# Kernel optimization log

Measured on AMD Instinct MI355X. Metric: run time of the kernel, lower is better.

## Reference

```python
import jax, jax.numpy as jnp
import numpy as np

B, T, D, H, O = 64, 512, 64, 512, 64

def setup_inputs() -> dict:
    key = jax.random.key(0)
    ks = jax.random.split(key, 12)
    s = lambda fan: 1.0 / np.sqrt(fan)
    return {
        "x": jax.random.normal(ks[0], (B, T, D), jnp.float32),
        "W_ih0": jax.random.normal(ks[1], (4 * H, D), jnp.float32) * s(D),
        "W_hh0": jax.random.normal(ks[2], (4 * H, H), jnp.float32) * s(H),
        "b_ih0": jax.random.normal(ks[3], (4 * H,), jnp.float32) * s(H),
        "b_hh0": jax.random.normal(ks[4], (4 * H,), jnp.float32) * s(H),
        "W_ih1": jax.random.normal(ks[5], (4 * H, H), jnp.float32) * s(H),
        "W_hh1": jax.random.normal(ks[6], (4 * H, H), jnp.float32) * s(H),
        "b_ih1": jax.random.normal(ks[7], (4 * H,), jnp.float32) * s(H),
        "b_hh1": jax.random.normal(ks[8], (4 * H,), jnp.float32) * s(H),
        "lin_w": jax.random.normal(ks[9], (O, H), jnp.float32) * s(H),
        "lin_b": jax.random.normal(ks[10], (O,), jnp.float32) * s(H),
    }

def _lstm_layer(x_seq, h0, c0, W_ih, W_hh, b_ih, b_hh):
    # Precompute input contribution for all timesteps: [B, T, 4H]
    xg = jnp.einsum('btd,gd->btg', x_seq, W_ih) + b_ih
    def step(carry, xg_t):
        h, c = carry
        gates = xg_t + h @ W_hh.T + b_hh  # [B, 4H]
        i, f, g, o = jnp.split(gates, 4, axis=-1)
        i = jax.nn.sigmoid(i); f = jax.nn.sigmoid(f)
        g = jnp.tanh(g); o = jax.nn.sigmoid(o)
        c = f * c + i * g  # eval mode: dropout mask is identity
        h = o * jnp.tanh(c)
        return (h, c), h
    (h, c), ys = jax.lax.scan(step, (h0, c0), jnp.swapaxes(xg, 0, 1))
    return jnp.swapaxes(ys, 0, 1), h, c

def reference(x, W_ih0, W_hh0, b_ih0, b_hh0, W_ih1, W_hh1, b_ih1, b_hh1, lin_w, lin_b):
    h = jnp.zeros((x.shape[0], H), x.dtype)
    c = jnp.zeros((x.shape[0], H), x.dtype)
    # NOTE: faithful to source — h/c are only zeroed before layer 0 and
    # carried into layer 1 as its initial state.
    y0, h, c = _lstm_layer(x, h, c, W_ih0, W_hh0, b_ih0, b_hh0)
    y1, h, c = _lstm_layer(y0, h, c, W_ih1, W_hh1, b_ih1, b_hh1)
    return h @ lin_w.T + lin_b  # [B, O]
```

## Files before the change

### kernel.cpp

```cpp
#include <hip/hip_runtime.h>

#define TSEQ 512

typedef unsigned short us8v __attribute__((ext_vector_type(8)));
typedef __bf16 bf16x8 __attribute__((ext_vector_type(8)));
typedef float f32x4 __attribute__((ext_vector_type(4)));
typedef unsigned u32x4 __attribute__((ext_vector_type(4)));

#define OFF_BIAS  0u
#define OFF_X16   16384u
#define OFF_W0    4210688u
#define OFF_W1    6569984u
#define OFF_Y0P   10764288u
#define OFF_RING0 44318720u
#define OFF_RING1 44580864u
#define OFF_HFIN  44843008u

static __device__ __forceinline__ unsigned short f2bf(float f) {
    unsigned u = __builtin_bit_cast(unsigned, f);
    u += 0x7fffu + ((u >> 16) & 1u);
    return (unsigned short)(u >> 16);
}
static __device__ __forceinline__ float sigmf(float x) { return 1.0f / (1.0f + __expf(-x)); }
static __device__ __forceinline__ float tanh_fast(float x) {
    float a = fabsf(x);
    float e = __expf(-2.0f * a);
    float t = (1.0f - e) / (1.0f + e);
    return copysignf(t, x);
}
static __device__ __forceinline__ f32x4 mfma16(us8v a, us8v b, f32x4 c) {
    return __builtin_amdgcn_mfma_f32_16x16x32_bf16(
        __builtin_bit_cast(bf16x8, a), __builtin_bit_cast(bf16x8, b), c, 0, 0, 0);
}
static __device__ __forceinline__ bool fresh8(u32x4 a,u32x4 b,u32x4 c,u32x4 d,
                                              u32x4 e,u32x4 f,u32x4 g,u32x4 h,unsigned ep) {
    unsigned x = (a[3]^ep)|(b[3]^ep)|(c[3]^ep)|(d[3]^ep)|(e[3]^ep)|(f[3]^ep)|(g[3]^ep)|(h[3]^ep);
    return __all((int)(x == 0u));
}

__global__ void setup_kernel(const float* __restrict__ x,
                             const float* __restrict__ wih0, const float* __restrict__ whh0,
                             const float* __restrict__ bih0, const float* __restrict__ bhh0,
                             const float* __restrict__ wih1, const float* __restrict__ whh1,
                             const float* __restrict__ bih1, const float* __restrict__ bhh1,
                             char* __restrict__ ws)
{
    unsigned idx = blockIdx.x * blockDim.x + threadIdx.x;
    unsigned stride = gridDim.x * blockDim.x;
    unsigned short* x16 = (unsigned short*)(ws + OFF_X16);
    unsigned short* w0  = (unsigned short*)(ws + OFF_W0);
    unsigned short* w1  = (unsigned short*)(ws + OFF_W1);
    float* bias = (float*)(ws + OFF_BIAS);
    const unsigned NX  = 64u*512u*64u;
    const unsigned NW0 = 2048u*576u;
    const unsigned NW1 = 2048u*1024u;
    const unsigned NT  = NX + NW0 + NW1 + 4096u;
    for (unsigned i = idx; i < NT; i += stride) {
        if (i < NX) {
            unsigned d = i & 63u, b = (i >> 6) & 63u, t = i >> 12;
            x16[i] = f2bf(x[((b << 9) + t) * 64u + d]);
        } else if (i < NX + NW0) {
            unsigned k = i - NX; unsigned r = k / 576u, c = k % 576u;
            float v = (c < 64u) ? wih0[r*64u + c] : whh0[r*512u + (c - 64u)];
            w0[k] = f2bf(v);
        } else if (i < NX + NW0 + NW1) {
            unsigned k = i - NX - NW0; unsigned r = k >> 10, c = k & 1023u;
            float v = (c < 512u) ? wih1[(r<<9) + c] : whh1[(r<<9) + (c - 512u)];
            w1[k] = f2bf(v);
        } else {
            unsigned k = i - NX - NW0 - NW1;
            float v = (k < 2048u) ? (bih0[k] + bhh0[k]) : (bih1[k-2048u] + bhh1[k-2048u]);
            bias[k] = v;
        }
    }
}

__launch_bounds__(256, 1)
__global__ void lstm_persist(char* __restrict__ ws)
{
    const int tid  = threadIdx.x;
    const int kq   = tid >> 6;
    const int lane = tid & 63;
    const int l15  = lane & 15;
    const int lhi  = lane >> 4;
    const int bg   = blockIdx.x & 3;
    const int hg   = blockIdx.x >> 2;

    const float* bias = (const float*)(ws + OFF_BIAS);
    const char*  x16  = ws + OFF_X16;
    char* y0p   = ws + OFF_Y0P;
    char* ring0 = ws + OFF_RING0;
    char* ring1 = ws + OFF_RING1;

    __shared__ __align__(16) char arena[86016];
    float* gsum   = (float*)arena;
    float* bias_l = (float*)(arena + 35840);

    if (tid < 64) bias_l[tid] = bias[(tid >> 4)*512 + hg*16 + (tid & 15)];

    float cst = 0.0f;
    const int b_ = tid >> 4, p_ = tid & 15;

    us8v A[4][8];
    {
        const char* w0p = ws + OFF_W0;
        #pragma unroll
        for (int m = 0; m < 4; ++m) {
            const char* base = w0p + (size_t)(m*512 + hg*16 + l15)*1152 + lhi*16;
            #pragma unroll
            for (int kk = 0; kk < 4; ++kk)
                A[m][kk] = *(const us8v*)(base + (2 + kq*4 + kk)*64);
            if (kq < 2) A[m][4] = *(const us8v*)(base + kq*64);
        }
    }
    __syncthreads();

    const int vo_a   = kq*8192 + (lhi>>1)*1024 + l15*64 + (lhi&1)*32;
    const int vo_b   = vo_a + 4096;
    const int vo_x   = l15*128 + (kq & 1)*64 + lhi*16;
    const int vo_y   = kq*4096 + (lhi>>1)*512 + l15*32 + (lhi&1)*16;
    const int vo_tag = b_*64 + (p_ & 3)*16;
    const int vo_pl  = b_*32 + (p_ & 1)*16;

    u32x4 c0,c1,c2,c3,c4,c5,c6,c7;

#define LOAD8(SB)                                                               \
    asm volatile(                                                               \
        "global_load_dwordx4 %0, %8, %10 sc0 sc1\n\t"                           \
        "global_load_dwordx4 %1, %8, %10 offset:16 sc0 sc1\n\t"                 \
        "global_load_dwordx4 %2, %8, %10 offset:2048 sc0 sc1\n\t"               \
        "global_load_dwordx4 %3, %8, %10 offset:2064 sc0 sc1\n\t"               \
        "global_load_dwordx4 %4, %9, %10 sc0 sc1\n\t"                           \
        "global_load_dwordx4 %5, %9, %10 offset:16 sc0 sc1\n\t"                 \
        "global_load_dwordx4 %6, %9, %10 offset:2048 sc0 sc1\n\t"               \
        "global_load_dwordx4 %7, %9, %10 offset:2064 sc0 sc1\n\t"               \
        "s_waitcnt vmcnt(0)"                                                    \
        : "=&v"(c0),"=&v"(c1),"=&v"(c2),"=&v"(c3),                              \
          "=&v"(c4),"=&v"(c5),"=&v"(c6),"=&v"(c7)                               \
        : "v"(vo_a), "v"(vo_b), "s"(SB) : "memory")

#define LOAD8X(SB, XR, SBX)                                                     \
    asm volatile(                                                               \
        "global_load_dwordx4 %8, %11, %12\n\t"                                  \
        "global_load_dwordx4 %0, %9, %13 sc0 sc1\n\t"                           \
        "global_load_dwordx4 %1, %9, %13 offset:16 sc0 sc1\n\t"                 \
        "global_load_dwordx4 %2, %9, %13 offset:2048 sc0 sc1\n\t"               \
        "global_load_dwordx4 %3, %9, %13 offset:2064 sc0 sc1\n\t"               \
        "global_load_dwordx4 %4, %10, %13 sc0 sc1\n\t"                          \
        "global_load_dwordx4 %5, %10, %13 offset:16 sc0 sc1\n\t"                \
        "global_load_dwordx4 %6, %10, %13 offset:2048 sc0 sc1\n\t"              \
        "global_load_dwordx4 %7, %10, %13 offset:2064 sc0 sc1\n\t"              \
        "s_waitcnt vmcnt(0)"                                                    \
        : "=&v"(c0),"=&v"(c1),"=&v"(c2),"=&v"(c3),                              \
          "=&v"(c4),"=&v"(c5),"=&v"(c6),"=&v"(c7), "=&v"(XR)                    \
        : "v"(vo_a), "v"(vo_b), "v"(vo_x), "s"(SBX), "s"(SB) : "memory")

#define LOAD8Y(SB, SBY)                                                         \
    asm volatile(                                                               \
        "global_load_dwordx4 %8, %14, %15\n\t"                                  \
        "global_load_dwordx4 %9, %14, %15 offset:1024\n\t"                      \
        "global_load_dwordx4 %10, %14, %15 offset:2048\n\t"                     \
        "global_load_dwordx4 %11, %14, %15 offset:3072\n\t"                     \
        "global_load_dwordx4 %0, %12, %16 sc0 sc1\n\t"                          \
        "global_load_dwordx4 %1, %12, %16 offset:16 sc0 sc1\n\t"                \
        "global_load_dwordx4 %2, %12, %16 offset:2048 sc0 sc1\n\t"              \
        "global_load_dwordx4 %3, %12, %16 offset:2064 sc0 sc1\n\t"              \
        "global_load_dwordx4 %4, %13, %16 sc0 sc1\n\t"                          \
        "global_load_dwordx4 %5, %13, %16 offset:16 sc0 sc1\n\t"                \
        "global_load_dwordx4 %6, %13, %16 offset:2048 sc0 sc1\n\t"              \
        "global_load_dwordx4 %7, %13, %16 offset:2064 sc0 sc1\n\t"              \
        "s_waitcnt vmcnt(0)"                                                    \
        : "=&v"(c0),"=&v"(c1),"=&v"(c2),"=&v"(c3),                              \
          "=&v"(c4),"=&v"(c5),"=&v"(c6),"=&v"(c7),                              \
          "=&v"(yr0),"=&v"(yr1),"=&v"(yr2),"=&v"(yr3)                           \
        : "v"(vo_a), "v"(vo_b), "v"(vo_y), "s"(SBY), "s"(SB) : "memory")

#define FRAG(a,b) __builtin_bit_cast(us8v, (u32x4){(a)[0],(a)[1],(b)[0],(b)[1]})

#define GSUM_WRITE(PAR)                                                           \
    do {                                                                          \
        float* gs_ = gsum + (PAR)*4352;                                           \
        _Pragma("unroll")                                                         \
        for (int m = 0; m < 4; ++m) {                                             \
            _Pragma("unroll")                                                     \
            for (int q = 0; q < 4; ++q)                                           \
                gs_[(m*16 + lhi*4 + q)*68 + kq*17 + l15] = acc[m][q];             \
        }                                                                         \
    } while (0)

#define ACT_STEP(PAR, EPS, SBTAG, DOPLAIN, SBPL)                                  \
    do {                                                                          \
        const float* gsr = gsum + (PAR)*4352;                                     \
        float g4[4];                                                              \
        _Pragma("unroll")                                                         \
        for (int g = 0; g < 4; ++g) {                                             \
            float s = bias_l[g*16 + p_];                                          \
            _Pragma("unroll")                                                     \
            for (int kk = 0; kk < 4; ++kk) s += gsr[(g*16 + p_)*68 + kk*17 + b_]; \
            g4[g] = s;                                                            \
        }                                                                         \
        float iv = sigmf(g4[0]), fv = sigmf(g4[1]);                               \
        float gv = tanh_fast(g4[2]), ov = sigmf(g4[3]);                           \
        cst = fv*cst + iv*gv;                                                     \
        float hh = ov * tanh_fast(cst);                                           \
        unsigned hv = f2bf(hh);                                                   \
        unsigned pk = (hv & 0xffffu) | (((unsigned)__shfl_xor((int)hv,1)) << 16); \
        int rbx = lane & 48;                                                      \
        unsigned Da = (unsigned)__shfl((int)pk, rbx + (p_&3)*4);                  \
        unsigned Db = (unsigned)__shfl((int)pk, rbx + (p_&3)*4 + 2);              \
        unsigned P0 = (unsigned)__shfl((int)pk, rbx + (p_&1)*8);                  \
        unsigned P1 = (unsigned)__shfl((int)pk, rbx + (p_&1)*8 + 2);              \
        unsigned P2 = (unsigned)__shfl((int)pk, rbx + (p_&1)*8 + 4);              \
        unsigned P3 = (unsigned)__shfl((int)pk, rbx + (p_&1)*8 + 6);              \
        if (p_ < 4) {                                                             \
            u32x4 tu = {Da, Db, 0u, (EPS)};                                       \
            asm volatile("global_store_dwordx4 %0, %1, %2 sc0 sc1"                \
                         :: "v"(vo_tag), "v"(tu), "s"(SBTAG) : "memory");         \
        }                                                                         \
        if ((DOPLAIN) && (p_ == 4 || p_ == 5)) {                                  \
            u32x4 pu = {P0, P1, P2, P3};                                          \
            asm volatile("global_store_dwordx4 %0, %1, %2 sc0 sc1"                \
                         :: "v"(vo_pl), "v"(pu), "s"(SBPL) : "memory");           \
        }                                                                         \
    } while (0)

    for (int t = 0; t < TSEQ; ++t) {
        const int par = t & 1;
        const char* sbx = x16 + (size_t)t*8192 + bg*2048;
        u32x4 xr;
        f32x4 acc[4] = {{0.f,0.f,0.f,0.f},{0.f,0.f,0.f,0.f},{0.f,0.f,0.f,0.f},{0.f,0.f,0.f,0.f}};
        if (t > 0) {
            const char* sbr = ring0 + ((size_t)((t-1)&1)*4 + bg)*32768;
            const unsigned ep = (unsigned)t;
            LOAD8X(sbr, xr, sbx);
            while (!fresh8(c0,c1,c2,c3,c4,c5,c6,c7, ep)) LOAD8(sbr);
            if (kq < 2) {
                #pragma unroll
                for (int m = 0; m < 4; ++m)
                    acc[m] = mfma16(A[m][4], __builtin_bit_cast(us8v, xr), acc[m]);
            }
            us8v h0 = FRAG(c0,c1), h1 = FRAG(c2,c3), h2 = FRAG(c4,c5), h3 = FRAG(c6,c7);
            #pragma unroll
            for (int m = 0; m < 4; ++m) acc[m] = mfma16(A[m][0], h0, acc[m]);
            #pragma unroll
            for (int m = 0; m < 4; ++m) acc[m] = mfma16(A[m][1], h1, acc[m]);
            #pragma unroll
            for (int m = 0; m < 4; ++m) acc[m] = mfma16(A[m][2], h2, acc[m]);
            #pragma unroll
            for (int m = 0; m < 4; ++m) acc[m] = mfma16(A[m][3], h3, acc[m]);
        } else {
            asm volatile("global_load_dwordx4 %0, %1, %2\n\ts_waitcnt vmcnt(0)"
                         : "=&v"(xr) : "v"(vo_x), "s"(sbx) : "memory");
            if (kq < 2) {
                #pragma unroll
                for (int m = 0; m < 4; ++m)
                    acc[m] = mfma16(A[m][4], __builtin_bit_cast(us8v, xr), acc[m]);
            }
        }
        GSUM_WRITE(par);
        __syncthreads();
        const char* sbt = ring0 + ((size_t)par*4 + bg)*32768 + hg*1024;
        const char* sbp = y0p + ((size_t)t*4 + bg)*16384 + hg*512;
        ACT_STEP(par, (unsigned)(t + 1), sbt, 1, sbp);
    }

    __syncthreads();
    {
        const char* w1p = ws + OFF_W1;
        #pragma unroll
        for (int m = 0; m < 4; ++m) {
            const char* base = w1p + (size_t)(m*512 + hg*16 + l15)*2048 + lhi*16;
            #pragma unroll
            for (int kk = 0; kk < 4; ++kk) {
                A[m][kk]     = *(const us8v*)(base + (kq*4 + kk)*64);
                A[m][kk + 4] = *(const us8v*)(base + (16 + kq*4 + kk)*64);
            }
        }
    }
    if (tid < 64) bias_l[tid] = bias[2048 + (tid >> 4)*512 + hg*16 + (tid & 15)];
    __syncthreads();

    for (int t = 0; t < TSEQ; ++t) {
        const int par = t & 1;
        const char* sby = y0p + ((size_t)t*4 + bg)*16384;
        const char* sbr = (t == 0) ? (ring0 + ((size_t)1*4 + bg)*32768)
                                   : (ring1 + ((size_t)((t-1)&1)*4 + bg)*32768);
        const unsigned ep = (unsigned)(512 + t);
        u32x4 yr0, yr1, yr2, yr3;
        LOAD8Y(sbr, sby);
        while (!fresh8(c0,c1,c2,c3,c4,c5,c6,c7, ep)) LOAD8(sbr);

        f32x4 acc[4] = {{0.f,0.f,0.f,0.f},{0.f,0.f,0.f,0.f},{0.f,0.f,0.f,0.f},{0.f,0.f,0.f,0.f}};
        #pragma unroll
        for (int m = 0; m < 4; ++m) acc[m] = mfma16(A[m][0], __builtin_bit_cast(us8v, yr0), acc[m]);
        #pragma unroll
        for (int m = 0; m < 4; ++m) acc[m] = mfma16(A[m][1], __builtin_bit_cast(us8v, yr1), acc[m]);
        #pragma unroll
        for (int m = 0; m < 4; ++m) acc[m] = mfma16(A[m][2], __builtin_bit_cast(us8v, yr2), acc[m]);
        #pragma unroll
        for (int m = 0; m < 4; ++m) acc[m] = mfma16(A[m][3], __builtin_bit_cast(us8v, yr3), acc[m]);
        {
            us8v h0 = FRAG(c0,c1), h1 = FRAG(c2,c3), h2 = FRAG(c4,c5), h3 = FRAG(c6,c7);
            #pragma unroll
            for (int m = 0; m < 4; ++m) acc[m] = mfma16(A[m][4], h0, acc[m]);
            #pragma unroll
            for (int m = 0; m < 4; ++m) acc[m] = mfma16(A[m][5], h1, acc[m]);
            #pragma unroll
            for (int m = 0; m < 4; ++m) acc[m] = mfma16(A[m][6], h2, acc[m]);
            #pragma unroll
            for (int m = 0; m < 4; ++m) acc[m] = mfma16(A[m][7], h3, acc[m]);
        }
        GSUM_WRITE(par);
        __syncthreads();
        const char* sbt = ring1 + ((size_t)par*4 + bg)*32768 + hg*1024;
        const char* sbp = ws + OFF_HFIN + ((size_t)bg*32 + hg)*512;
        ACT_STEP(par, (unsigned)(513 + t), sbt, (t == 511), sbp);
    }
#undef LOAD8
#undef LOAD8X
#undef LOAD8Y
#undef FRAG
#undef GSUM_WRITE
#undef ACT_STEP
}

__global__ void final_linear(const char* __restrict__ ws,
                             const float* __restrict__ linw, const float* __restrict__ linb,
                             float* __restrict__ out)
{
    __shared__ float hrow[512];
    int b = blockIdx.x;
    int o = threadIdx.x;
    int bg = b >> 4, bl = b & 15;
    const char* src = ws + OFF_HFIN + ((size_t)bg*32 + (o >> 1))*512 + bl*32 + (o & 1)*16;
    {
        us8v v = *(const us8v*)src;
        #pragma unroll
        for (int p = 0; p < 8; ++p)
            hrow[o*8+p] = __builtin_bit_cast(float, ((unsigned)v[p]) << 16);
    }
    __syncthreads();
    float acc = linb[o];
    const float* wrow = linw + o*512;
    #pragma unroll 8
    for (int k = 0; k < 512; ++k) acc += hrow[k] * wrow[k];
    out[b*64 + o] = acc;
}

extern "C" void kernel_launch(void* const* d_in, const int* in_sizes, int n_in,
                              void* d_out, int out_size, void* d_ws, size_t ws_size,
                              hipStream_t stream)
{
    const float* x    = (const float*)d_in[0];
    const float* wih0 = (const float*)d_in[1];
    const float* whh0 = (const float*)d_in[2];
    const float* bih0 = (const float*)d_in[3];
    const float* bhh0 = (const float*)d_in[4];
    const float* wih1 = (const float*)d_in[5];
    const float* whh1 = (const float*)d_in[6];
    const float* bih1 = (const float*)d_in[7];
    const float* bih1_ = bih1;  (void)bih1_;
    const float* bhh1 = (const float*)d_in[8];
    const float* linw = (const float*)d_in[9];
    const float* linb = (const float*)d_in[10];
    char* ws = (char*)d_ws;

    (void)hipMemsetAsync(ws + OFF_RING0, 0, 262144u*2 + 65536u, stream);
    hipLaunchKernelGGL(setup_kernel, dim3(1024), dim3(256), 0, stream,
                       x, wih0, whh0, bih0, bhh0, wih1, whh1, bih1, bhh1, ws);
    hipLaunchKernelGGL(lstm_persist, dim3(128), dim3(256), 0, stream, ws);
    hipLaunchKernelGGL(final_linear, dim3(64), dim3(64), 0, stream,
                       ws, linw, linb, (float*)d_out);
}
```

Before: 2.489 ms.

## Halve persistent grid and replace tagged ring polling with per-group flag counters

The persistent LSTM kernel moves from 128 to 64 blocks, with each block owning 32 hidden units (8 MFMA row tiles) instead of 16. Cross-block hidden-state exchange no longer polls epoch tags embedded in every 16-byte payload. It now uses plain h buffers plus a small per-batch-group flag array, polled with a tight inline-asm loop, and layer-0 outputs are read directly from y0p. This is meant to cut the number of blocks that must synchronise each timestep and the polling traffic, at the cost of twice as much MFMA and activation work per block and more registers for the weights.

After: 3.195 ms. 28.4% more time.

```diff
diff --git a/kernel.cpp b/kernel.cpp
--- a/kernel.cpp
+++ b/kernel.cpp
@@ -12,9 +12,8 @@
 #define OFF_W0    4210688u
 #define OFF_W1    6569984u
 #define OFF_Y0P   10764288u
-#define OFF_RING0 44318720u
-#define OFF_RING1 44580864u
-#define OFF_HFIN  44843008u
+#define OFF_RING1 44318720u
+#define OFF_FLAGS 44449792u
 
 static __device__ __forceinline__ unsigned short f2bf(float f) {
     unsigned u = __builtin_bit_cast(unsigned, f);
@@ -32,11 +31,7 @@
     return __builtin_amdgcn_mfma_f32_16x16x32_bf16(
         __builtin_bit_cast(bf16x8, a), __builtin_bit_cast(bf16x8, b), c, 0, 0, 0);
 }
-static __device__ __forceinline__ bool fresh8(u32x4 a,u32x4 b,u32x4 c,u32x4 d,
-                                              u32x4 e,u32x4 f,u32x4 g,u32x4 h,unsigned ep) {
-    unsigned x = (a[3]^ep)|(b[3]^ep)|(c[3]^ep)|(d[3]^ep)|(e[3]^ep)|(f[3]^ep)|(g[3]^ep)|(h[3]^ep);
-    return __all((int)(x == 0u));
-}
+static __device__ __forceinline__ us8v asb(u32x4 v) { return __builtin_bit_cast(us8v, v); }
 
 __global__ void setup_kernel(const float* __restrict__ x,
                              const float* __restrict__ wih0, const float* __restrict__ whh0,
@@ -89,24 +84,27 @@
     const float* bias = (const float*)(ws + OFF_BIAS);
     const char*  x16  = ws + OFF_X16;
     char* y0p   = ws + OFF_Y0P;
-    char* ring0 = ws + OFF_RING0;
     char* ring1 = ws + OFF_RING1;
+    char* flags = ws + OFF_FLAGS;
 
     __shared__ __align__(16) char arena[86016];
     float* gsum   = (float*)arena;
-    float* bias_l = (float*)(arena + 35840);
-
-    if (tid < 64) bias_l[tid] = bias[(tid >> 4)*512 + hg*16 + (tid & 15)];
-
-    float cst = 0.0f;
-    const int b_ = tid >> 4, p_ = tid & 15;
-
-    us8v A[4][8];
+    float* bias_l = (float*)(arena + 70656);
+    unsigned* wcnt = (unsigned*)(arena + 71680);
+
+    if (tid == 0) { wcnt[0] = 0u; wcnt[1] = 0u; }
+    if (tid < 128) bias_l[tid] = bias[(tid >> 5)*512 + hg*32 + (tid & 31)];
+
+    const int b_ = tid >> 4, p0 = (tid & 15) * 2;
+    float cs0 = 0.0f, cs1 = 0.0f;
+
+    us8v A[8][8];
     {
         const char* w0p = ws + OFF_W0;
         #pragma unroll
-        for (int m = 0; m < 4; ++m) {
-            const char* base = w0p + (size_t)(m*512 + hg*16 + l15)*1152 + lhi*16;
+        for (int m = 0; m < 8; ++m) {
+            const char* base = w0p
+                + (size_t)((m >> 1)*512 + hg*32 + (m & 1)*16 + l15)*1152 + lhi*16;
             #pragma unroll
             for (int kk = 0; kk < 4; ++kk)
                 A[m][kk] = *(const us8v*)(base + (2 + kq*4 + kk)*64);
@@ -115,161 +113,168 @@
     }
     __syncthreads();
 
-    const int vo_a   = kq*8192 + (lhi>>1)*1024 + l15*64 + (lhi&1)*32;
-    const int vo_b   = vo_a + 4096;
-    const int vo_x   = l15*128 + (kq & 1)*64 + lhi*16;
-    const int vo_y   = kq*4096 + (lhi>>1)*512 + l15*32 + (lhi&1)*16;
-    const int vo_tag = b_*64 + (p_ & 3)*16;
-    const int vo_pl  = b_*32 + (p_ & 1)*16;
-
-    u32x4 c0,c1,c2,c3,c4,c5,c6,c7;
-
-#define LOAD8(SB)                                                               \
+    const int vo_h = kq*4096 + l15*64 + lhi*16;
+    const int vo_x = (bg*16 + l15)*128 + (kq & 1)*64 + lhi*16;
+    const char* fp = flags + bg*2048 + (lane & 15)*128;
+    const char* fq = flags + bg*2048 + hg*128;
+
+    u32x4 xr, yr0, yr1, yr2, yr3, h0, h1, h2, h3;
+
+#define POLL_L0(SBX, EP)                                                        \
+    do { unsigned pf0_, pf1_, ep_ = (EP);                                       \
     asm volatile(                                                               \
-        "global_load_dwordx4 %0, %8, %10 sc0 sc1\n\t"                           \
-        "global_load_dwordx4 %1, %8, %10 offset:16 sc0 sc1\n\t"                 \
-        "global_load_dwordx4 %2, %8, %10 offset:2048 sc0 sc1\n\t"               \
-        "global_load_dwordx4 %3, %8, %10 offset:2064 sc0 sc1\n\t"               \
-        "global_load_dwordx4 %4, %9, %10 sc0 sc1\n\t"                           \
-        "global_load_dwordx4 %5, %9, %10 offset:16 sc0 sc1\n\t"                 \
-        "global_load_dwordx4 %6, %9, %10 offset:2048 sc0 sc1\n\t"               \
-        "global_load_dwordx4 %7, %9, %10 offset:2064 sc0 sc1\n\t"               \
+        "global_load_dwordx4 %0, %3, %4\n\t"                                    \
+        "global_load_dword %1, %5, off sc0 sc1\n\t"                             \
+        "global_load_dword %2, %5, off sc0 sc1\n\t"                             \
+        "1:\n\t"                                                                \
+        "s_waitcnt vmcnt(1)\n\t"                                                \
+        "v_cmp_lt_u32 vcc, %1, %6\n\t"                                          \
+        "s_cbranch_vccz 2f\n\t"                                                 \
+        "global_load_dword %1, %5, off sc0 sc1\n\t"                             \
+        "s_waitcnt vmcnt(1)\n\t"                                                \
+        "v_cmp_lt_u32 vcc, %2, %6\n\t"                                          \
+        "s_cbranch_vccz 2f\n\t"                                                 \
+        "global_load_dword %2, %5, off sc0 sc1\n\t"                             \
+        "s_branch 1b\n\t"                                                       \
+        "2:\n\t"                                                                \
         "s_waitcnt vmcnt(0)"                                                    \
-        : "=&v"(c0),"=&v"(c1),"=&v"(c2),"=&v"(c3),                              \
-          "=&v"(c4),"=&v"(c5),"=&v"(c6),"=&v"(c7)                               \
-        : "v"(vo_a), "v"(vo_b), "s"(SB) : "memory")
-
-#define LOAD8X(SB, XR, SBX)                                                     \
+        : "=&v"(xr), "=&v"(pf0_), "=&v"(pf1_)                                   \
+        : "v"(vo_x), "s"(SBX), "v"(fp), "v"(ep_)                                \
+        : "vcc", "memory"); } while (0)
+
+#define POLL_L1(SBY, EP)                                                        \
+    do { unsigned pf0_, pf1_, ep_ = (EP);                                       \
     asm volatile(                                                               \
-        "global_load_dwordx4 %8, %11, %12\n\t"                                  \
-        "global_load_dwordx4 %0, %9, %13 sc0 sc1\n\t"                           \
-        "global_load_dwordx4 %1, %9, %13 offset:16 sc0 sc1\n\t"                 \
-        "global_load_dwordx4 %2, %9, %13 offset:2048 sc0 sc1\n\t"               \
-        "global_load_dwordx4 %3, %9, %13 offset:2064 sc0 sc1\n\t"               \
-        "global_load_dwordx4 %4, %10, %13 sc0 sc1\n\t"                          \
-        "global_load_dwordx4 %5, %10, %13 offset:16 sc0 sc1\n\t"                \
-        "global_load_dwordx4 %6, %10, %13 offset:2048 sc0 sc1\n\t"              \
-        "global_load_dwordx4 %7, %10, %13 offset:2064 sc0 sc1\n\t"              \
+        "global_load_dwordx4 %0, %6, %7\n\t"                                    \
+        "global_load_dwordx4 %1, %6, %7 offset:1024\n\t"                        \
+        "global_load_dwordx4 %2, %6, %7 offset:2048\n\t"                        \
+        "global_load_dwordx4 %3, %6, %7 offset:3072\n\t"                        \
+        "global_load_dword %4, %8, off sc0 sc1\n\t"                             \
+        "global_load_dword %5, %8, off sc0 sc1\n\t"                             \
+        "1:\n\t"                                                                \
+        "s_waitcnt vmcnt(1)\n\t"                                                \
+        "v_cmp_lt_u32 vcc, %4, %9\n\t"                                          \
+        "s_cbranch_vccz 2f\n\t"                                                 \
+        "global_load_dword %4, %8, off sc0 sc1\n\t"                             \
+        "s_waitcnt vmcnt(1)\n\t"                                                \
+        "v_cmp_lt_u32 vcc, %5, %9\n\t"                                          \
+        "s_cbranch_vccz 2f\n\t"                                                 \
+        "global_load_dword %5, %8, off sc0 sc1\n\t"                             \
+        "s_branch 1b\n\t"                                                       \
+        "2:\n\t"                                                                \
         "s_waitcnt vmcnt(0)"                                                    \
-        : "=&v"(c0),"=&v"(c1),"=&v"(c2),"=&v"(c3),                              \
-          "=&v"(c4),"=&v"(c5),"=&v"(c6),"=&v"(c7), "=&v"(XR)                    \
-        : "v"(vo_a), "v"(vo_b), "v"(vo_x), "s"(SBX), "s"(SB) : "memory")
-
-#define LOAD8Y(SB, SBY)                                                         \
+        : "=&v"(yr0), "=&v"(yr1), "=&v"(yr2), "=&v"(yr3), "=&v"(pf0_), "=&v"(pf1_) \
+        : "v"(vo_h), "s"(SBY), "v"(fp), "v"(ep_)                                \
+        : "vcc", "memory"); } while (0)
+
+#define LOADH4(SB)                                                              \
     asm volatile(                                                               \
-        "global_load_dwordx4 %8, %14, %15\n\t"                                  \
-        "global_load_dwordx4 %9, %14, %15 offset:1024\n\t"                      \
-        "global_load_dwordx4 %10, %14, %15 offset:2048\n\t"                     \
-        "global_load_dwordx4 %11, %14, %15 offset:3072\n\t"                     \
-        "global_load_dwordx4 %0, %12, %16 sc0 sc1\n\t"                          \
-        "global_load_dwordx4 %1, %12, %16 offset:16 sc0 sc1\n\t"                \
-        "global_load_dwordx4 %2, %12, %16 offset:2048 sc0 sc1\n\t"              \
-        "global_load_dwordx4 %3, %12, %16 offset:2064 sc0 sc1\n\t"              \
-        "global_load_dwordx4 %4, %13, %16 sc0 sc1\n\t"                          \
-        "global_load_dwordx4 %5, %13, %16 offset:16 sc0 sc1\n\t"                \
-        "global_load_dwordx4 %6, %13, %16 offset:2048 sc0 sc1\n\t"              \
-        "global_load_dwordx4 %7, %13, %16 offset:2064 sc0 sc1\n\t"              \
+        "global_load_dwordx4 %0, %4, %5\n\t"                                    \
+        "global_load_dwordx4 %1, %4, %5 offset:1024\n\t"                        \
+        "global_load_dwordx4 %2, %4, %5 offset:2048\n\t"                        \
+        "global_load_dwordx4 %3, %4, %5 offset:3072\n\t"                        \
         "s_waitcnt vmcnt(0)"                                                    \
-        : "=&v"(c0),"=&v"(c1),"=&v"(c2),"=&v"(c3),                              \
-          "=&v"(c4),"=&v"(c5),"=&v"(c6),"=&v"(c7),                              \
-          "=&v"(yr0),"=&v"(yr1),"=&v"(yr2),"=&v"(yr3)                           \
-        : "v"(vo_a), "v"(vo_b), "v"(vo_y), "s"(SBY), "s"(SB) : "memory")
-
-#define FRAG(a,b) __builtin_bit_cast(us8v, (u32x4){(a)[0],(a)[1],(b)[0],(b)[1]})
-
-#define GSUM_WRITE(PAR)                                                           \
-    do {                                                                          \
-        float* gs_ = gsum + (PAR)*4352;                                           \
-        _Pragma("unroll")                                                         \
-        for (int m = 0; m < 4; ++m) {                                             \
-            _Pragma("unroll")                                                     \
-            for (int q = 0; q < 4; ++q)                                           \
-                gs_[(m*16 + lhi*4 + q)*68 + kq*17 + l15] = acc[m][q];             \
-        }                                                                         \
-    } while (0)
-
-#define ACT_STEP(PAR, EPS, SBTAG, DOPLAIN, SBPL)                                  \
-    do {                                                                          \
-        const float* gsr = gsum + (PAR)*4352;                                     \
-        float g4[4];                                                              \
-        _Pragma("unroll")                                                         \
-        for (int g = 0; g < 4; ++g) {                                             \
-            float s = bias_l[g*16 + p_];                                          \
-            _Pragma("unroll")                                                     \
-            for (int kk = 0; kk < 4; ++kk) s += gsr[(g*16 + p_)*68 + kk*17 + b_]; \
-            g4[g] = s;                                                            \
-        }                                                                         \
-        float iv = sigmf(g4[0]), fv = sigmf(g4[1]);                               \
-        float gv = tanh_fast(g4[2]), ov = sigmf(g4[3]);                           \
-        cst = fv*cst + iv*gv;                                                     \
-        float hh = ov * tanh_fast(cst);                                           \
-        unsigned hv = f2bf(hh);                                                   \
-        unsigned pk = (hv & 0xffffu) | (((unsigned)__shfl_xor((int)hv,1)) << 16); \
-        int rbx = lane & 48;                                                      \
-        unsigned Da = (unsigned)__shfl((int)pk, rbx + (p_&3)*4);                  \
-        unsigned Db = (unsigned)__shfl((int)pk, rbx + (p_&3)*4 + 2);              \
-        unsigned P0 = (unsigned)__shfl((int)pk, rbx + (p_&1)*8);                  \
-        unsigned P1 = (unsigned)__shfl((int)pk, rbx + (p_&1)*8 + 2);              \
-        unsigned P2 = (unsigned)__shfl((int)pk, rbx + (p_&1)*8 + 4);              \
-        unsigned P3 = (unsigned)__shfl((int)pk, rbx + (p_&1)*8 + 6);              \
-        if (p_ < 4) {                                                             \
-            u32x4 tu = {Da, Db, 0u, (EPS)};                                       \
-            asm volatile("global_store_dwordx4 %0, %1, %2 sc0 sc1"                \
-                         :: "v"(vo_tag), "v"(tu), "s"(SBTAG) : "memory");         \
-        }                                                                         \
-        if ((DOPLAIN) && (p_ == 4 || p_ == 5)) {                                  \
-            u32x4 pu = {P0, P1, P2, P3};                                          \
-            asm volatile("global_store_dwordx4 %0, %1, %2 sc0 sc1"                \
-                         :: "v"(vo_pl), "v"(pu), "s"(SBPL) : "memory");           \
-        }                                                                         \
+        : "=&v"(h0),"=&v"(h1),"=&v"(h2),"=&v"(h3)                               \
+        : "v"(vo_h), "s"(SB) : "memory")
+#define LOADR4(SB)                                                              \
+    asm volatile(                                                               \
+        "global_load_dwordx4 %0, %4, %5 sc0 sc1\n\t"                            \
+        "global_load_dwordx4 %1, %4, %5 offset:1024 sc0 sc1\n\t"                \
+        "global_load_dwordx4 %2, %4, %5 offset:2048 sc0 sc1\n\t"                \
+        "global_load_dwordx4 %3, %4, %5 offset:3072 sc0 sc1\n\t"                \
+        "s_waitcnt vmcnt(0)"                                                    \
+        : "=&v"(h0),"=&v"(h1),"=&v"(h2),"=&v"(h3)                               \
+        : "v"(vo_h), "s"(SB) : "memory")
+
+#define GSUM_WRITE(PAR)                                                         \
+    do { float* gs_ = gsum + (PAR)*8832;                                        \
+        _Pragma("unroll")                                                       \
+        for (int m = 0; m < 8; ++m) {                                           \
+            _Pragma("unroll")                                                   \
+            for (int q = 0; q < 4; ++q)                                         \
+                gs_[(m*16 + lhi*4 + q)*69 + kq*17 + l15] = acc[m][q];           \
+        } } while (0)
+
+#define ACT_STEP(PAR, EPS, SBSL)                                                \
+    do {                                                                        \
+        const float* gsr = gsum + (PAR)*8832;                                   \
+        float g4a[4], g4b[4];                                                   \
+        _Pragma("unroll")                                                       \
+        for (int g = 0; g < 4; ++g) {                                           \
+            float sa = bias_l[g*32 + p0], sb2 = bias_l[g*32 + p0 + 1];          \
+            _Pragma("unroll")                                                   \
+            for (int kk = 0; kk < 4; ++kk) {                                    \
+                sa  += gsr[(g*32 + p0)*69     + kk*17 + b_];                    \
+                sb2 += gsr[(g*32 + p0 + 1)*69 + kk*17 + b_];                    \
+            }                                                                   \
+            g4a[g] = sa; g4b[g] = sb2;                                          \
+        }                                                                       \
+        float iv = sigmf(g4a[0]), fv = sigmf(g4a[1]);                           \
+        float gv = tanh_fast(g4a[2]), ov = sigmf(g4a[3]);                       \
+        cs0 = fv*cs0 + iv*gv;                                                   \
+        float ha = ov * tanh_fast(cs0);                                         \
+        iv = sigmf(g4b[0]); fv = sigmf(g4b[1]);                                 \
+        gv = tanh_fast(g4b[2]); ov = sigmf(g4b[3]);                             \
+        cs1 = fv*cs1 + iv*gv;                                                   \
+        float hb = ov * tanh_fast(cs1);                                         \
+        unsigned pk = ((unsigned)f2bf(ha)) | (((unsigned)f2bf(hb)) << 16);      \
+        const char* dst_ = (SBSL) + b_*64 + p0*2;                               \
+        asm volatile("global_store_dword %0, %1, off sc0 sc1"                   \
+                     :: "v"(dst_), "v"(pk) : "memory");                         \
+        asm volatile("s_waitcnt vmcnt(0)" ::: "memory");                        \
+        if (lane == 0) {                                                        \
+            unsigned prev_ = __hip_atomic_fetch_add(&wcnt[PAR], 1u,             \
+                                __ATOMIC_RELAXED, __HIP_MEMORY_SCOPE_WORKGROUP);\
+            if (prev_ == 3u) {                                                  \
+                __hip_atomic_store(&wcnt[PAR], 0u,                              \
+                                __ATOMIC_RELAXED, __HIP_MEMORY_SCOPE_WORKGROUP);\
+                unsigned ep_ = (EPS);                                           \
+                asm volatile("global_store_dword %0, %1, off sc0 sc1"           \
+                             :: "v"(fq), "v"(ep_) : "memory");                  \
+            }                                                                   \
+        }                                                                       \
     } while (0)
 
     for (int t = 0; t < TSEQ; ++t) {
         const int par = t & 1;
-        const char* sbx = x16 + (size_t)t*8192 + bg*2048;
-        u32x4 xr;
-        f32x4 acc[4] = {{0.f,0.f,0.f,0.f},{0.f,0.f,0.f,0.f},{0.f,0.f,0.f,0.f},{0.f,0.f,0.f,0.f}};
+        const char* sbx = x16 + (size_t)t*8192;
+        f32x4 acc[8] = {{0.f,0.f,0.f,0.f},{0.f,0.f,0.f,0.f},{0.f,0.f,0.f,0.f},{0.f,0.f,0.f,0.f},
+                        {0.f,0.f,0.f,0.f},{0.f,0.f,0.f,0.f},{0.f,0.f,0.f,0.f},{0.f,0.f,0.f,0.f}};
         if (t > 0) {
-            const char* sbr = ring0 + ((size_t)((t-1)&1)*4 + bg)*32768;
-            const unsigned ep = (unsigned)t;
-            LOAD8X(sbr, xr, sbx);
-            while (!fresh8(c0,c1,c2,c3,c4,c5,c6,c7, ep)) LOAD8(sbr);
+            POLL_L0(sbx, (unsigned)t);
+            LOADH4(y0p + ((size_t)(t-1)*4 + bg)*16384);
             if (kq < 2) {
                 #pragma unroll
-                for (int m = 0; m < 4; ++m)
-                    acc[m] = mfma16(A[m][4], __builtin_bit_cast(us8v, xr), acc[m]);
+                for (int m = 0; m < 8; ++m) acc[m] = mfma16(A[m][4], asb(xr), acc[m]);
             }
-            us8v h0 = FRAG(c0,c1), h1 = FRAG(c2,c3), h2 = FRAG(c4,c5), h3 = FRAG(c6,c7);
-            #pragma unroll
-            for (int m = 0; m < 4; ++m) acc[m] = mfma16(A[m][0], h0, acc[m]);
-            #pragma unroll
-            for (int m = 0; m < 4; ++m) acc[m] = mfma16(A[m][1], h1, acc[m]);
-            #pragma unroll
-            for (int m = 0; m < 4; ++m) acc[m] = mfma16(A[m][2], h2, acc[m]);
-            #pragma unroll
-            for (int m = 0; m < 4; ++m) acc[m] = mfma16(A[m][3], h3, acc[m]);
+            #pragma unroll
+            for (int m = 0; m < 8; ++m) acc[m] = mfma16(A[m][0], asb(h0), acc[m]);
+            #pragma unroll
+            for (int m = 0; m < 8; ++m) acc[m] = mfma16(A[m][1], asb(h1), acc[m]);
+            #pragma unroll
+            for (int m = 0; m < 8; ++m) acc[m] = mfma16(A[m][2], asb(h2), acc[m]);
+            #pragma unroll
+            for (int m = 0; m < 8; ++m) acc[m] = mfma16(A[m][3], asb(h3), acc[m]);
         } else {
             asm volatile("global_load_dwordx4 %0, %1, %2\n\ts_waitcnt vmcnt(0)"
                          : "=&v"(xr) : "v"(vo_x), "s"(sbx) : "memory");
             if (kq < 2) {
                 #pragma unroll
-                for (int m = 0; m < 4; ++m)
-                    acc[m] = mfma16(A[m][4], __builtin_bit_cast(us8v, xr), acc[m]);
+                for (int m = 0; m < 8; ++m) acc[m] = mfma16(A[m][4], asb(xr), acc[m]);
             }
         }
         GSUM_WRITE(par);
         __syncthreads();
-        const char* sbt = ring0 + ((size_t)par*4 + bg)*32768 + hg*1024;
-        const char* sbp = y0p + ((size_t)t*4 + bg)*16384 + hg*512;
-        ACT_STEP(par, (unsigned)(t + 1), sbt, 1, sbp);
+        ACT_STEP(par, (unsigned)(t + 1), y0p + ((size_t)t*4 + bg)*16384 + hg*1024);
     }
 
     __syncthreads();
     {
         const char* w1p = ws + OFF_W1;
         #pragma unroll
-        for (int m = 0; m < 4; ++m) {
-            const char* base = w1p + (size_t)(m*512 + hg*16 + l15)*2048 + lhi*16;
+        for (int m = 0; m < 8; ++m) {
+            const char* base = w1p
+                + (size_t)((m >> 1)*512 + hg*32 + (m & 1)*16 + l15)*2048 + lhi*16;
             #pragma unroll
             for (int kk = 0; kk < 4; ++kk) {
                 A[m][kk]     = *(const us8v*)(base + (kq*4 + kk)*64);
@@ -277,49 +282,43 @@
             }
         }
     }
-    if (tid < 64) bias_l[tid] = bias[2048 + (tid >> 4)*512 + hg*16 + (tid & 15)];
+    if (tid < 128) bias_l[tid] = bias[2048 + (tid >> 5)*512 + hg*32 + (tid & 31)];
     __syncthreads();
 
     for (int t = 0; t < TSEQ; ++t) {
         const int par = t & 1;
         const char* sby = y0p + ((size_t)t*4 + bg)*16384;
-        const char* sbr = (t == 0) ? (ring0 + ((size_t)1*4 + bg)*32768)
-                                   : (ring1 + ((size_t)((t-1)&1)*4 + bg)*32768);
-        const unsigned ep = (unsigned)(512 + t);
-        u32x4 yr0, yr1, yr2, yr3;
-        LOAD8Y(sbr, sby);
-        while (!fresh8(c0,c1,c2,c3,c4,c5,c6,c7, ep)) LOAD8(sbr);
-
-        f32x4 acc[4] = {{0.f,0.f,0.f,0.f},{0.f,0.f,0.f,0.f},{0.f,0.f,0.f,0.f},{0.f,0.f,0.f,0.f}};
-        #pragma unroll
-        for (int m = 0; m < 4; ++m) acc[m] = mfma16(A[m][0], __builtin_bit_cast(us8v, yr0), acc[m]);
-        #pragma unroll
-        for (int m = 0; m < 4; ++m) acc[m] = mfma16(A[m][1], __builtin_bit_cast(us8v, yr1), acc[m]);
-        #pragma unroll
-        for (int m = 0; m < 4; ++m) acc[m] = mfma16(A[m][2], __builtin_bit_cast(us8v, yr2), acc[m]);
-        #pragma unroll
-        for (int m = 0; m < 4; ++m) acc[m] = mfma16(A[m][3], __builtin_bit_cast(us8v, yr3), acc[m]);
-        {
-            us8v h0 = FRAG(c0,c1), h1 = FRAG(c2,c3), h2 = FRAG(c4,c5), h3 = FRAG(c6,c7);
-            #pragma unroll
-            for (int m = 0; m < 4; ++m) acc[m] = mfma16(A[m][4], h0, acc[m]);
-            #pragma unroll
-            for (int m = 0; m < 4; ++m) acc[m] = mfma16(A[m][5], h1, acc[m]);
-            #pragma unroll
-            for (int m = 0; m < 4; ++m) acc[m] = mfma16(A[m][6], h2, acc[m]);
-            #pragma unroll
-            for (int m = 0; m < 4; ++m) acc[m] = mfma16(A[m][7], h3, acc[m]);
-        }
+        POLL_L1(sby, (unsigned)(512 + t));
+        if (t == 0) { LOADR4(y0p + ((size_t)511*4 + bg)*16384); }
+        else        { LOADR4(ring1 + ((size_t)((t-1) & 1)*4 + bg)*16384); }
+
+        f32x4 acc[8] = {{0.f,0.f,0.f,0.f},{0.f,0.f,0.f,0.f},{0.f,0.f,0.f,0.f},{0.f,0.f,0.f,0.f},
+                        {0.f,0.f,0.f,0.f},{0.f,0.f,0.f,0.f},{0.f,0.f,0.f,0.f},{0.f,0.f,0.f,0.f}};
+        #pragma unroll
+        for (int m = 0; m < 8; ++m) acc[m] = mfma16(A[m][0], asb(yr0), acc[m]);
+        #pragma unroll
+        for (int m = 0; m < 8; ++m) acc[m] = mfma16(A[m][1], asb(yr1), acc[m]);
+        #pragma unroll
+        for (int m = 0; m < 8; ++m) acc[m] = mfma16(A[m][2], asb(yr2), acc[m]);
+        #pragma unroll
+        for (int m = 0; m < 8; ++m) acc[m] = mfma16(A[m][3], asb(yr3), acc[m]);
+        #pragma unroll
+        for (int m = 0; m < 8; ++m) acc[m] = mfma16(A[m][4], asb(h0), acc[m]);
+        #pragma unroll
+        for (int m = 0; m < 8; ++m) acc[m] = mfma16(A[m][5], asb(h1), acc[m]);
+        #pragma unroll
+        for (int m = 0; m < 8; ++m) acc[m] = mfma16(A[m][6], asb(h2), acc[m]);
+        #pragma unroll
+        for (int m = 0; m < 8; ++m) acc[m] = mfma16(A[m][7], asb(h3), acc[m]);
+
         GSUM_WRITE(par);
         __syncthreads();
-        const char* sbt = ring1 + ((size_t)par*4 + bg)*32768 + hg*1024;
-        const char* sbp = ws + OFF_HFIN + ((size_t)bg*32 + hg)*512;
-        ACT_STEP(par, (unsigned)(513 + t), sbt, (t == 511), sbp);
-    }
-#undef LOAD8
-#undef LOAD8X
-#undef LOAD8Y
-#undef FRAG
+        ACT_STEP(par, (unsigned)(513 + t), ring1 + ((size_t)par*4 + bg)*16384 + hg*1024);
+    }
+#undef POLL_L0
+#undef POLL_L1
+#undef LOADH4
+#undef LOADR4
 #undef GSUM_WRITE
 #undef ACT_STEP
 }
@@ -332,7 +331,8 @@
     int b = blockIdx.x;
     int o = threadIdx.x;
     int bg = b >> 4, bl = b & 15;
-    const char* src = ws + OFF_HFIN + ((size_t)bg*32 + (o >> 1))*512 + bl*32 + (o & 1)*16;
+    const char* src = ws + OFF_RING1 + ((size_t)(4 + bg))*16384
+                         + (o >> 2)*1024 + bl*64 + (o & 3)*16;
     {
         us8v v = *(const us8v*)src;
         #pragma unroll
@@ -359,16 +359,15 @@
     const float* wih1 = (const float*)d_in[5];
     const float* whh1 = (const float*)d_in[6];
     const float* bih1 = (const float*)d_in[7];
-    const float* bih1_ = bih1;  (void)bih1_;
     const float* bhh1 = (const float*)d_in[8];
     const float* linw = (const float*)d_in[9];
     const float* linb = (const float*)d_in[10];
     char* ws = (char*)d_ws;
 
-    (void)hipMemsetAsync(ws + OFF_RING0, 0, 262144u*2 + 65536u, stream);
+    (void)hipMemsetAsync(ws + OFF_FLAGS, 0, 8192, stream);
     hipLaunchKernelGGL(setup_kernel, dim3(1024), dim3(256), 0, stream,
                        x, wih0, whh0, bih0, bhh0, wih1, whh1, bih1, bhh1, ws);
-    hipLaunchKernelGGL(lstm_persist, dim3(128), dim3(256), 0, stream, ws);
+    hipLaunchKernelGGL(lstm_persist, dim3(64), dim3(256), 0, stream, ws);
     hipLaunchKernelGGL(final_linear, dim3(64), dim3(64), 0, stream,
                        ws, linw, linb, (float*)d_out);
 }
```
